# Performance work log

Hardware: AMD Instinct MI355X
Metric: run time of the kernel (lower is better)

Reference implementation:

```python
import jax, jax.numpy as jnp
import numpy as np

NUM_NODES = 100000
OUT_CHANNELS = 32
NUM_EDGES = 3200000


def setup_inputs() -> dict:
    key = jax.random.key(0)
    k1, k2, k3 = jax.random.split(key, 3)
    edge_index = jax.random.randint(k1, (2, NUM_EDGES), 0, NUM_NODES, dtype=jnp.int64)
    # nn.Linear init: weight [out, in], uniform(-1/sqrt(in), 1/sqrt(in))
    bound = 1.0 / np.sqrt(NUM_NODES)
    W = jax.random.uniform(k2, (OUT_CHANNELS, NUM_NODES), jnp.float32, -bound, bound)
    b = jax.random.uniform(k3, (OUT_CHANNELS,), jnp.float32, -bound, bound)
    return {"edge_index": edge_index, "W": W, "b": b}


def reference(edge_index, W, b):
    # LINK forward: A = sparse COO [N, num_nodes] with 1.0 per edge (duplicates sum),
    # logits = A @ W.T + b. Implemented as gather + segment_sum (no dense A).
    row = edge_index[0]
    col = edge_index[1]
    row = row - row.min()  # faithful to `row = row - row.min()`
    gathered = jnp.take(W.T, col, axis=0)  # [E, out_channels]
    logits = jax.ops.segment_sum(gathered, row, num_segments=NUM_NODES)  # [N, out]
    return logits + b
```

## Files before the change

kernel.cpp:

```cpp
#include <hip/hip_runtime.h>

#define NUM_NODES 100000
#define OUT_CH 32
#define NUM_EDGES 3200000

#define RPB 128
#define NB 782
#define NBG 783
#define CAP2 5120
#define FTPB 1024
#define TRB 782
#define BINB 250
#define TILE 12800
#define TPB 512

static __device__ __forceinline__ unsigned short f32_to_bf16_rne(float f) {
    unsigned u = __float_as_uint(f);
    unsigned r = u + 0x7FFFu + ((u >> 16) & 1u);
    return (unsigned short)(r >> 16);
}
static __device__ __forceinline__ float bf16_to_f32(unsigned short h) {
    return __uint_as_float(((unsigned)h) << 16);
}

__global__ void __launch_bounds__(FTPB)
fused_pre(const float* __restrict__ W, ushort4* __restrict__ Wt,
          const int* __restrict__ edge, int* __restrict__ partmin,
          int* __restrict__ bcount, unsigned int* __restrict__ bin) {
    int bk = blockIdx.x;
    int t  = threadIdx.x;
    if (bk < TRB) {
        __shared__ float tile[32][129];
        int tx = t & 127, ty = t >> 7;
        int colBase = bk * 128;
        int col = colBase + tx;
        if (col < NUM_NODES) {
            #pragma unroll
            for (int k = 0; k < 4; k++) {
                int c = ty + 8 * k;
                tile[c][tx] = W[(size_t)c * NUM_NODES + col];
            }
        }
        __syncthreads();
        int lc = t >> 3, q = t & 7;
        int ocol = colBase + lc;
        if (ocol < NUM_NODES) {
            ushort4 o;
            o.x = f32_to_bf16_rne(tile[q * 4 + 0][lc]);
            o.y = f32_to_bf16_rne(tile[q * 4 + 1][lc]);
            o.z = f32_to_bf16_rne(tile[q * 4 + 2][lc]);
            o.w = f32_to_bf16_rne(tile[q * 4 + 3][lc]);
            Wt[(size_t)ocol * 8 + q] = o;
        }
    } else {
        int mb = bk - TRB;
        __shared__ int cnt[NB];
        __shared__ int cur[NB];
        __shared__ int wm[16];
        for (int i = t; i < NB; i += FTPB) cnt[i] = 0;
        __syncthreads();
        int base = mb * TILE;
        int rm = 0x7fffffff;
        for (int o = t; o < TILE; o += FTPB) {
            int r = edge[base + o];
            rm = min(rm, r);
            atomicAdd(&cnt[r >> 7], 1);
        }
        #pragma unroll
        for (int off = 32; off > 0; off >>= 1) rm = min(rm, __shfl_down(rm, off, 64));
        if ((t & 63) == 0) wm[t >> 6] = rm;
        __syncthreads();
        if (t == 0) {
            int m = wm[0];
            #pragma unroll
            for (int w = 1; w < 16; w++) m = min(m, wm[w]);
            partmin[mb] = m;
        }
        for (int i = t; i < NB; i += FTPB)
            cur[i] = cnt[i] ? atomicAdd(&bcount[i], cnt[i]) : 0;
        __syncthreads();
        for (int o = t; o < TILE; o += FTPB) {
            int r = edge[base + o];
            int c = edge[NUM_EDGES + base + o];
            int b = r >> 7;
            int pos = atomicAdd(&cur[b], 1);
            if (pos < CAP2)
                bin[(size_t)b * CAP2 + pos] = ((unsigned)(r & 127) << 17) | (unsigned)c;
        }
    }
}

__global__ void __launch_bounds__(TPB)
bucket_gather(const unsigned int* __restrict__ bin, const int* __restrict__ bcount,
              const int* __restrict__ partmin,
              const ushort4* __restrict__ Wt, const float* __restrict__ b,
              float* __restrict__ out) {
    __shared__ int cnt2[RPB * 8];
    __shared__ int cur2[RPB * 8];
    __shared__ int rowstart[RPB];
    __shared__ int rowcnt[RPB];
    __shared__ int scn[RPB];
    __shared__ int lcol[CAP2];
    __shared__ int wmin[8];
    __shared__ int rminS;

    int t = threadIdx.x;
    int bk = blockIdx.x;
    int pm = (t < BINB) ? partmin[t] : 0x7fffffff;
    #pragma unroll
    for (int off = 32; off > 0; off >>= 1) pm = min(pm, __shfl_down(pm, off, 64));
    if ((t & 63) == 0) wmin[t >> 6] = pm;

    int n = (bk < NB) ? bcount[bk] : 0;
    if (n > CAP2) n = CAP2;
    const unsigned int* mybin = bin + (size_t)bk * CAP2;

    for (int i = t; i < RPB * 8; i += TPB) cnt2[i] = 0;
    __syncthreads();
    if (t == 0) {
        int m = wmin[0];
        #pragma unroll
        for (int w = 1; w < 8; w++) m = min(m, wmin[w]);
        rminS = m;
    }

    for (int i = t; i < n; i += TPB) {
        unsigned int p = mybin[i];
        int lr  = p >> 17;
        int seg = (p & 0x1FFFF) >> 14;
        atomicAdd(&cnt2[(lr << 3) | seg], 1);
    }
    __syncthreads();

    if (t < RPB) {
        int s = 0;
        #pragma unroll
        for (int k = 0; k < 8; k++) s += cnt2[(t << 3) | k];
        rowcnt[t] = s;
        scn[t] = s;
    }
    __syncthreads();
    for (int off = 1; off < RPB; off <<= 1) {
        int v = (t < RPB && t >= off) ? scn[t - off] : 0;
        __syncthreads();
        if (t < RPB) scn[t] += v;
        __syncthreads();
    }
    if (t < RPB) {
        int rs = scn[t] - rowcnt[t];
        rowstart[t] = rs;
        int run = rs;
        #pragma unroll
        for (int k = 0; k < 8; k++) { cur2[(t << 3) | k] = run; run += cnt2[(t << 3) | k]; }
    }
    __syncthreads();

    for (int i = t; i < n; i += TPB) {
        unsigned int p = mybin[i];
        int lr = p >> 17;
        int c  = p & 0x1FFFF;
        int pos = atomicAdd(&cur2[(lr << 3) | (c >> 14)], 1);
        lcol[pos] = c;
    }
    __syncthreads();

    int g   = t >> 3;
    int sub = t & 7;
    float4 bias = ((const float4*)b)[sub];
    int rmin = rminS;
    int lrA = g, lrB = g + 64;
    int outA = bk * RPB + lrA - rmin;
    int outB = bk * RPB + lrB - rmin;
    bool vA = (unsigned)outA < NUM_NODES;
    bool vB = (unsigned)outB < NUM_NODES;
    int iA = rowstart[lrA], eA = iA + rowcnt[lrA];
    int iB = rowstart[lrB], eB = iB + rowcnt[lrB];
    if (!vA) { iA = eA = 0; }
    if (!vB) { iB = eB = 0; }
    float4 accA = bias, accB = bias;
    int nPair = min(eA - iA, eB - iB);
    int k = 0;
    for (; k + 2 <= nPair; k += 2) {
        int cA0 = lcol[iA + k],     cB0 = lcol[iB + k];
        int cA1 = lcol[iA + k + 1], cB1 = lcol[iB + k + 1];
        ushort4 wA0 = Wt[(size_t)cA0 * 8 + sub];
        ushort4 wB0 = Wt[(size_t)cB0 * 8 + sub];
        ushort4 wA1 = Wt[(size_t)cA1 * 8 + sub];
        ushort4 wB1 = Wt[(size_t)cB1 * 8 + sub];
        accA.x += bf16_to_f32(wA0.x) + bf16_to_f32(wA1.x);
        accA.y += bf16_to_f32(wA0.y) + bf16_to_f32(wA1.y);
        accA.z += bf16_to_f32(wA0.z) + bf16_to_f32(wA1.z);
        accA.w += bf16_to_f32(wA0.w) + bf16_to_f32(wA1.w);
        accB.x += bf16_to_f32(wB0.x) + bf16_to_f32(wB1.x);
        accB.y += bf16_to_f32(wB0.y) + bf16_to_f32(wB1.y);
        accB.z += bf16_to_f32(wB0.z) + bf16_to_f32(wB1.z);
        accB.w += bf16_to_f32(wB0.w) + bf16_to_f32(wB1.w);
    }
    for (; k < nPair; k++) {
        ushort4 wA = Wt[(size_t)lcol[iA + k] * 8 + sub];
        ushort4 wB = Wt[(size_t)lcol[iB + k] * 8 + sub];
        accA.x += bf16_to_f32(wA.x); accA.y += bf16_to_f32(wA.y);
        accA.z += bf16_to_f32(wA.z); accA.w += bf16_to_f32(wA.w);
        accB.x += bf16_to_f32(wB.x); accB.y += bf16_to_f32(wB.y);
        accB.z += bf16_to_f32(wB.z); accB.w += bf16_to_f32(wB.w);
    }
    iA += nPair; iB += nPair;
    for (; iA < eA; iA++) {
        ushort4 w = Wt[(size_t)lcol[iA] * 8 + sub];
        accA.x += bf16_to_f32(w.x); accA.y += bf16_to_f32(w.y);
        accA.z += bf16_to_f32(w.z); accA.w += bf16_to_f32(w.w);
    }
    for (; iB < eB; iB++) {
        ushort4 w = Wt[(size_t)lcol[iB] * 8 + sub];
        accB.x += bf16_to_f32(w.x); accB.y += bf16_to_f32(w.y);
        accB.z += bf16_to_f32(w.z); accB.w += bf16_to_f32(w.w);
    }
    if (vA) ((float4*)out)[(size_t)outA * 8 + sub] = accA;
    if (vB) ((float4*)out)[(size_t)outB * 8 + sub] = accB;
}

extern "C" void kernel_launch(void* const* d_in, const int* in_sizes, int n_in,
                              void* d_out, int out_size, void* d_ws, size_t ws_size,
                              hipStream_t stream) {
    const int*   edge = (const int*)d_in[0];
    const float* W    = (const float*)d_in[1];
    const float* b    = (const float*)d_in[2];
    float* out = (float*)d_out;

    char* ws = (char*)d_ws;
    int*          partmin = (int*)ws;
    int*          bcount  = (int*)(ws + 1024);
    ushort4*      Wt      = (ushort4*)(ws + 8192);
    unsigned int* bin     = (unsigned int*)(ws + 6422528);

    hipMemsetAsync(bcount, 0, NBG * sizeof(int), stream);
    fused_pre<<<TRB + BINB, FTPB, 0, stream>>>(W, Wt, edge, partmin, bcount, bin);
    bucket_gather<<<NBG, TPB, 0, stream>>>(bin, bcount, partmin, Wt, b, out);
}
```

Measured before the change: 181.6 us.

## Fuse preprocessing and bucket gather into one persistent cooperative kernel

Merges the transpose/binning kernel and the bucket-gather kernel into a single cooperative persistent kernel. Blocks loop over work items and are separated by a hand-rolled grid barrier on an atomic counter, with shared memory overlaid through a union. Binning now runs with 512-thread blocks over 512 slices instead of 250 tiles of 1024 threads. The aim is to remove the second launch and its gap. In exchange it adds a grid-wide spin barrier and caps the grid size, which may cut parallelism in the gather phase and in the transpose/binning split.

```diff
diff --git a/kernel.cpp b/kernel.cpp
--- a/kernel.cpp
+++ b/kernel.cpp
@@ -8,11 +8,10 @@
 #define NB 782
 #define NBG 783
 #define CAP2 5120
-#define FTPB 1024
+#define TPB 512
 #define TRB 782
-#define BINB 250
-#define TILE 12800
-#define TPB 512
+#define BINS 512
+#define SLICE 6250
 
 static __device__ __forceinline__ unsigned short f32_to_bf16_rne(float f) {
     unsigned u = __float_as_uint(f);
@@ -23,200 +22,217 @@
     return __uint_as_float(((unsigned)h) << 16);
 }
 
-__global__ void __launch_bounds__(FTPB)
-fused_pre(const float* __restrict__ W, ushort4* __restrict__ Wt,
-          const int* __restrict__ edge, int* __restrict__ partmin,
-          int* __restrict__ bcount, unsigned int* __restrict__ bin) {
-    int bk = blockIdx.x;
-    int t  = threadIdx.x;
-    if (bk < TRB) {
-        __shared__ float tile[32][129];
-        int tx = t & 127, ty = t >> 7;
-        int colBase = bk * 128;
-        int col = colBase + tx;
-        if (col < NUM_NODES) {
-            #pragma unroll
-            for (int k = 0; k < 4; k++) {
-                int c = ty + 8 * k;
-                tile[c][tx] = W[(size_t)c * NUM_NODES + col];
-            }
-        }
-        __syncthreads();
-        int lc = t >> 3, q = t & 7;
-        int ocol = colBase + lc;
-        if (ocol < NUM_NODES) {
-            ushort4 o;
-            o.x = f32_to_bf16_rne(tile[q * 4 + 0][lc]);
-            o.y = f32_to_bf16_rne(tile[q * 4 + 1][lc]);
-            o.z = f32_to_bf16_rne(tile[q * 4 + 2][lc]);
-            o.w = f32_to_bf16_rne(tile[q * 4 + 3][lc]);
-            Wt[(size_t)ocol * 8 + q] = o;
+struct TransLds { float tile[32][129]; };
+struct BinLds   { int cnt[NB]; int cur[NB]; int wm[8]; };
+struct GatherLds {
+    int cnt2[RPB * 8]; int cur2[RPB * 8];
+    int rowstart[RPB]; int rowcnt[RPB]; int scn[RPB];
+    int lcol[CAP2]; int wmin[8];
+};
+union AllLds { TransLds tr; BinLds bn; GatherLds g; };
+
+static __device__ __forceinline__ void grid_barrier(int* bar, int t) {
+    __syncthreads();
+    if (t == 0) {
+        __hip_atomic_fetch_add(bar, 1, __ATOMIC_RELEASE, __HIP_MEMORY_SCOPE_AGENT);
+        while (__hip_atomic_load(bar, __ATOMIC_RELAXED, __HIP_MEMORY_SCOPE_AGENT) < (int)gridDim.x)
+            __builtin_amdgcn_s_sleep(2);
+        __builtin_amdgcn_fence(__ATOMIC_ACQUIRE, "agent");
+    }
+    __syncthreads();
+}
+
+__global__ void __launch_bounds__(TPB, 8)
+link_all(const float* __restrict__ W, ushort4* Wt,
+         const int* __restrict__ edge, int* partmin,
+         int* bcount, unsigned int* bin,
+         const float* __restrict__ bv, float* __restrict__ out,
+         int* bar) {
+    __shared__ AllLds u;
+    int bk   = blockIdx.x;
+    int t    = threadIdx.x;
+    int grid = gridDim.x;
+    int tb0  = (grid >= BINS + 256) ? BINS : (grid >> 1);
+
+    if (bk < tb0) {
+        for (int sl = bk; sl < BINS; sl += tb0) {
+            for (int i = t; i < NB; i += TPB) u.bn.cnt[i] = 0;
+            __syncthreads();
+            int base = sl * SLICE;
+            int rm = 0x7fffffff;
+            for (int o = t; o < SLICE; o += TPB) {
+                int r = edge[base + o];
+                rm = min(rm, r);
+                atomicAdd(&u.bn.cnt[r >> 7], 1);
+            }
+            #pragma unroll
+            for (int off = 32; off > 0; off >>= 1) rm = min(rm, __shfl_down(rm, off, 64));
+            if ((t & 63) == 0) u.bn.wm[t >> 6] = rm;
+            __syncthreads();
+            if (t == 0) {
+                int m = u.bn.wm[0];
+                #pragma unroll
+                for (int w = 1; w < TPB / 64; w++) m = min(m, u.bn.wm[w]);
+                partmin[sl] = m;
+            }
+            for (int i = t; i < NB; i += TPB)
+                u.bn.cur[i] = u.bn.cnt[i] ? atomicAdd(&bcount[i], u.bn.cnt[i]) : 0;
+            __syncthreads();
+            for (int o = t; o < SLICE; o += TPB) {
+                int r = edge[base + o];
+                int c = edge[NUM_EDGES + base + o];
+                int b = r >> 7;
+                int pos = atomicAdd(&u.bn.cur[b], 1);
+                if (pos < CAP2)
+                    bin[(size_t)b * CAP2 + pos] = ((unsigned)(r & 127) << 17) | (unsigned)c;
+            }
+            __syncthreads();
         }
     } else {
-        int mb = bk - TRB;
-        __shared__ int cnt[NB];
-        __shared__ int cur[NB];
-        __shared__ int wm[16];
-        for (int i = t; i < NB; i += FTPB) cnt[i] = 0;
-        __syncthreads();
-        int base = mb * TILE;
-        int rm = 0x7fffffff;
-        for (int o = t; o < TILE; o += FTPB) {
-            int r = edge[base + o];
-            rm = min(rm, r);
-            atomicAdd(&cnt[r >> 7], 1);
-        }
-        #pragma unroll
-        for (int off = 32; off > 0; off >>= 1) rm = min(rm, __shfl_down(rm, off, 64));
-        if ((t & 63) == 0) wm[t >> 6] = rm;
-        __syncthreads();
-        if (t == 0) {
-            int m = wm[0];
-            #pragma unroll
-            for (int w = 1; w < 16; w++) m = min(m, wm[w]);
-            partmin[mb] = m;
-        }
-        for (int i = t; i < NB; i += FTPB)
-            cur[i] = cnt[i] ? atomicAdd(&bcount[i], cnt[i]) : 0;
-        __syncthreads();
-        for (int o = t; o < TILE; o += FTPB) {
-            int r = edge[base + o];
-            int c = edge[NUM_EDGES + base + o];
-            int b = r >> 7;
-            int pos = atomicAdd(&cur[b], 1);
-            if (pos < CAP2)
-                bin[(size_t)b * CAP2 + pos] = ((unsigned)(r & 127) << 17) | (unsigned)c;
-        }
-    }
-}
-
-__global__ void __launch_bounds__(TPB)
-bucket_gather(const unsigned int* __restrict__ bin, const int* __restrict__ bcount,
-              const int* __restrict__ partmin,
-              const ushort4* __restrict__ Wt, const float* __restrict__ b,
-              float* __restrict__ out) {
-    __shared__ int cnt2[RPB * 8];
-    __shared__ int cur2[RPB * 8];
-    __shared__ int rowstart[RPB];
-    __shared__ int rowcnt[RPB];
-    __shared__ int scn[RPB];
-    __shared__ int lcol[CAP2];
-    __shared__ int wmin[8];
-    __shared__ int rminS;
-
-    int t = threadIdx.x;
-    int bk = blockIdx.x;
-    int pm = (t < BINB) ? partmin[t] : 0x7fffffff;
+        int tstride = grid - tb0;
+        for (int tb = bk - tb0; tb < TRB; tb += tstride) {
+            int tx = t & 127, ty = t >> 7;
+            int colBase = tb * 128;
+            int col = colBase + tx;
+            if (col < NUM_NODES) {
+                #pragma unroll
+                for (int k = 0; k < 8; k++) {
+                    int c = ty + 4 * k;
+                    u.tr.tile[c][tx] = W[(size_t)c * NUM_NODES + col];
+                }
+            }
+            __syncthreads();
+            #pragma unroll
+            for (int s = 0; s < 2; s++) {
+                int o  = s * TPB + t;
+                int lc = o >> 3, q = o & 7;
+                int ocol = colBase + lc;
+                if (ocol < NUM_NODES) {
+                    ushort4 w;
+                    w.x = f32_to_bf16_rne(u.tr.tile[q * 4 + 0][lc]);
+                    w.y = f32_to_bf16_rne(u.tr.tile[q * 4 + 1][lc]);
+                    w.z = f32_to_bf16_rne(u.tr.tile[q * 4 + 2][lc]);
+                    w.w = f32_to_bf16_rne(u.tr.tile[q * 4 + 3][lc]);
+                    Wt[(size_t)ocol * 8 + q] = w;
+                }
+            }
+            __syncthreads();
+        }
+    }
+    grid_barrier(bar, t);
+
+    int pm = (t < BINS) ? partmin[t] : 0x7fffffff;
     #pragma unroll
     for (int off = 32; off > 0; off >>= 1) pm = min(pm, __shfl_down(pm, off, 64));
-    if ((t & 63) == 0) wmin[t >> 6] = pm;
-
-    int n = (bk < NB) ? bcount[bk] : 0;
-    if (n > CAP2) n = CAP2;
-    const unsigned int* mybin = bin + (size_t)bk * CAP2;
-
-    for (int i = t; i < RPB * 8; i += TPB) cnt2[i] = 0;
-    __syncthreads();
-    if (t == 0) {
-        int m = wmin[0];
-        #pragma unroll
-        for (int w = 1; w < 8; w++) m = min(m, wmin[w]);
-        rminS = m;
-    }
-
-    for (int i = t; i < n; i += TPB) {
-        unsigned int p = mybin[i];
-        int lr  = p >> 17;
-        int seg = (p & 0x1FFFF) >> 14;
-        atomicAdd(&cnt2[(lr << 3) | seg], 1);
-    }
-    __syncthreads();
-
-    if (t < RPB) {
-        int s = 0;
-        #pragma unroll
-        for (int k = 0; k < 8; k++) s += cnt2[(t << 3) | k];
-        rowcnt[t] = s;
-        scn[t] = s;
-    }
-    __syncthreads();
-    for (int off = 1; off < RPB; off <<= 1) {
-        int v = (t < RPB && t >= off) ? scn[t - off] : 0;
-        __syncthreads();
-        if (t < RPB) scn[t] += v;
-        __syncthreads();
-    }
-    if (t < RPB) {
-        int rs = scn[t] - rowcnt[t];
-        rowstart[t] = rs;
-        int run = rs;
-        #pragma unroll
-        for (int k = 0; k < 8; k++) { cur2[(t << 3) | k] = run; run += cnt2[(t << 3) | k]; }
-    }
-    __syncthreads();
-
-    for (int i = t; i < n; i += TPB) {
-        unsigned int p = mybin[i];
-        int lr = p >> 17;
-        int c  = p & 0x1FFFF;
-        int pos = atomicAdd(&cur2[(lr << 3) | (c >> 14)], 1);
-        lcol[pos] = c;
-    }
-    __syncthreads();
-
-    int g   = t >> 3;
-    int sub = t & 7;
-    float4 bias = ((const float4*)b)[sub];
-    int rmin = rminS;
-    int lrA = g, lrB = g + 64;
-    int outA = bk * RPB + lrA - rmin;
-    int outB = bk * RPB + lrB - rmin;
-    bool vA = (unsigned)outA < NUM_NODES;
-    bool vB = (unsigned)outB < NUM_NODES;
-    int iA = rowstart[lrA], eA = iA + rowcnt[lrA];
-    int iB = rowstart[lrB], eB = iB + rowcnt[lrB];
-    if (!vA) { iA = eA = 0; }
-    if (!vB) { iB = eB = 0; }
-    float4 accA = bias, accB = bias;
-    int nPair = min(eA - iA, eB - iB);
-    int k = 0;
-    for (; k + 2 <= nPair; k += 2) {
-        int cA0 = lcol[iA + k],     cB0 = lcol[iB + k];
-        int cA1 = lcol[iA + k + 1], cB1 = lcol[iB + k + 1];
-        ushort4 wA0 = Wt[(size_t)cA0 * 8 + sub];
-        ushort4 wB0 = Wt[(size_t)cB0 * 8 + sub];
-        ushort4 wA1 = Wt[(size_t)cA1 * 8 + sub];
-        ushort4 wB1 = Wt[(size_t)cB1 * 8 + sub];
-        accA.x += bf16_to_f32(wA0.x) + bf16_to_f32(wA1.x);
-        accA.y += bf16_to_f32(wA0.y) + bf16_to_f32(wA1.y);
-        accA.z += bf16_to_f32(wA0.z) + bf16_to_f32(wA1.z);
-        accA.w += bf16_to_f32(wA0.w) + bf16_to_f32(wA1.w);
-        accB.x += bf16_to_f32(wB0.x) + bf16_to_f32(wB1.x);
-        accB.y += bf16_to_f32(wB0.y) + bf16_to_f32(wB1.y);
-        accB.z += bf16_to_f32(wB0.z) + bf16_to_f32(wB1.z);
-        accB.w += bf16_to_f32(wB0.w) + bf16_to_f32(wB1.w);
-    }
-    for (; k < nPair; k++) {
-        ushort4 wA = Wt[(size_t)lcol[iA + k] * 8 + sub];
-        ushort4 wB = Wt[(size_t)lcol[iB + k] * 8 + sub];
-        accA.x += bf16_to_f32(wA.x); accA.y += bf16_to_f32(wA.y);
-        accA.z += bf16_to_f32(wA.z); accA.w += bf16_to_f32(wA.w);
-        accB.x += bf16_to_f32(wB.x); accB.y += bf16_to_f32(wB.y);
-        accB.z += bf16_to_f32(wB.z); accB.w += bf16_to_f32(wB.w);
-    }
-    iA += nPair; iB += nPair;
-    for (; iA < eA; iA++) {
-        ushort4 w = Wt[(size_t)lcol[iA] * 8 + sub];
-        accA.x += bf16_to_f32(w.x); accA.y += bf16_to_f32(w.y);
-        accA.z += bf16_to_f32(w.z); accA.w += bf16_to_f32(w.w);
-    }
-    for (; iB < eB; iB++) {
-        ushort4 w = Wt[(size_t)lcol[iB] * 8 + sub];
-        accB.x += bf16_to_f32(w.x); accB.y += bf16_to_f32(w.y);
-        accB.z += bf16_to_f32(w.z); accB.w += bf16_to_f32(w.w);
-    }
-    if (vA) ((float4*)out)[(size_t)outA * 8 + sub] = accA;
-    if (vB) ((float4*)out)[(size_t)outB * 8 + sub] = accB;
+    if ((t & 63) == 0) u.g.wmin[t >> 6] = pm;
+    __syncthreads();
+    int rmin = u.g.wmin[0];
+    #pragma unroll
+    for (int w = 1; w < TPB / 64; w++) rmin = min(rmin, u.g.wmin[w]);
+    __syncthreads();
+
+    for (int gb = bk; gb < NBG; gb += grid) {
+        int n = (gb < NB) ? bcount[gb] : 0;
+        if (n > CAP2) n = CAP2;
+        const unsigned int* mybin = bin + (size_t)gb * CAP2;
+
+        for (int i = t; i < RPB * 8; i += TPB) u.g.cnt2[i] = 0;
+        __syncthreads();
+
+        for (int i = t; i < n; i += TPB) {
+            unsigned int p = mybin[i];
+            int lr  = p >> 17;
+            int seg = (p & 0x1FFFF) >> 14;
+            atomicAdd(&u.g.cnt2[(lr << 3) | seg], 1);
+        }
+        __syncthreads();
+
+        if (t < RPB) {
+            int s = 0;
+            #pragma unroll
+            for (int k = 0; k < 8; k++) s += u.g.cnt2[(t << 3) | k];
+            u.g.rowcnt[t] = s;
+            u.g.scn[t] = s;
+        }
+        __syncthreads();
+        for (int off = 1; off < RPB; off <<= 1) {
+            int v = (t < RPB && t >= off) ? u.g.scn[t - off] : 0;
+            __syncthreads();
+            if (t < RPB) u.g.scn[t] += v;
+            __syncthreads();
+        }
+        if (t < RPB) {
+            int rs = u.g.scn[t] - u.g.rowcnt[t];
+            u.g.rowstart[t] = rs;
+            int run = rs;
+            #pragma unroll
+            for (int k = 0; k < 8; k++) { u.g.cur2[(t << 3) | k] = run; run += u.g.cnt2[(t << 3) | k]; }
+        }
+        __syncthreads();
+
+        for (int i = t; i < n; i += TPB) {
+            unsigned int p = mybin[i];
+            int lr = p >> 17;
+            int c  = p & 0x1FFFF;
+            int pos = atomicAdd(&u.g.cur2[(lr << 3) | (c >> 14)], 1);
+            u.g.lcol[pos] = c;
+        }
+        __syncthreads();
+
+        int g   = t >> 3;
+        int sub = t & 7;
+        float4 bias = ((const float4*)bv)[sub];
+        int lrA = g, lrB = g + 64;
+        int outA = gb * RPB + lrA - rmin;
+        int outB = gb * RPB + lrB - rmin;
+        bool vA = (unsigned)outA < NUM_NODES;
+        bool vB = (unsigned)outB < NUM_NODES;
+        int iA = u.g.rowstart[lrA], eA = iA + u.g.rowcnt[lrA];
+        int iB = u.g.rowstart[lrB], eB = iB + u.g.rowcnt[lrB];
+        if (!vA) { iA = eA = 0; }
+        if (!vB) { iB = eB = 0; }
+        float4 accA = bias, accB = bias;
+        int nPair = min(eA - iA, eB - iB);
+        int k = 0;
+        for (; k + 2 <= nPair; k += 2) {
+            int cA0 = u.g.lcol[iA + k],     cB0 = u.g.lcol[iB + k];
+            int cA1 = u.g.lcol[iA + k + 1], cB1 = u.g.lcol[iB + k + 1];
+            ushort4 wA0 = Wt[(size_t)cA0 * 8 + sub];
+            ushort4 wB0 = Wt[(size_t)cB0 * 8 + sub];
+            ushort4 wA1 = Wt[(size_t)cA1 * 8 + sub];
+            ushort4 wB1 = Wt[(size_t)cB1 * 8 + sub];
+            accA.x += bf16_to_f32(wA0.x) + bf16_to_f32(wA1.x);
+            accA.y += bf16_to_f32(wA0.y) + bf16_to_f32(wA1.y);
+            accA.z += bf16_to_f32(wA0.z) + bf16_to_f32(wA1.z);
+            accA.w += bf16_to_f32(wA0.w) + bf16_to_f32(wA1.w);
+            accB.x += bf16_to_f32(wB0.x) + bf16_to_f32(wB1.x);
+            accB.y += bf16_to_f32(wB0.y) + bf16_to_f32(wB1.y);
+            accB.z += bf16_to_f32(wB0.z) + bf16_to_f32(wB1.z);
+            accB.w += bf16_to_f32(wB0.w) + bf16_to_f32(wB1.w);
+        }
+        for (; k < nPair; k++) {
+            ushort4 wA = Wt[(size_t)u.g.lcol[iA + k] * 8 + sub];
+            ushort4 wB = Wt[(size_t)u.g.lcol[iB + k] * 8 + sub];
+            accA.x += bf16_to_f32(wA.x); accA.y += bf16_to_f32(wA.y);
+            accA.z += bf16_to_f32(wA.z); accA.w += bf16_to_f32(wA.w);
+            accB.x += bf16_to_f32(wB.x); accB.y += bf16_to_f32(wB.y);
+            accB.z += bf16_to_f32(wB.z); accB.w += bf16_to_f32(wB.w);
+        }
+        iA += nPair; iB += nPair;
+        for (; iA < eA; iA++) {
+            ushort4 w = Wt[(size_t)u.g.lcol[iA] * 8 + sub];
+            accA.x += bf16_to_f32(w.x); accA.y += bf16_to_f32(w.y);
+            accA.z += bf16_to_f32(w.z); accA.w += bf16_to_f32(w.w);
+        }
+        for (; iB < eB; iB++) {
+            ushort4 w = Wt[(size_t)u.g.lcol[iB] * 8 + sub];
+            accB.x += bf16_to_f32(w.x); accB.y += bf16_to_f32(w.y);
+            accB.z += bf16_to_f32(w.z); accB.w += bf16_to_f32(w.w);
+        }
+        if (vA) ((float4*)out)[(size_t)outA * 8 + sub] = accA;
+        if (vB) ((float4*)out)[(size_t)outB * 8 + sub] = accB;
+        __syncthreads();
+    }
 }
 
 extern "C" void kernel_launch(void* const* d_in, const int* in_sizes, int n_in,
@@ -228,12 +244,24 @@
     float* out = (float*)d_out;
 
     char* ws = (char*)d_ws;
-    int*          partmin = (int*)ws;
-    int*          bcount  = (int*)(ws + 1024);
+    int*          bar     = (int*)ws;
+    int*          partmin = (int*)(ws + 1024);
+    int*          bcount  = (int*)(ws + 4096);
     ushort4*      Wt      = (ushort4*)(ws + 8192);
     unsigned int* bin     = (unsigned int*)(ws + 6422528);
 
-    hipMemsetAsync(bcount, 0, NBG * sizeof(int), stream);
-    fused_pre<<<TRB + BINB, FTPB, 0, stream>>>(W, Wt, edge, partmin, bcount, bin);
-    bucket_gather<<<NBG, TPB, 0, stream>>>(bin, bcount, partmin, Wt, b, out);
-}
+    static int bpc = 0;
+    if (bpc == 0) {
+        hipOccupancyMaxActiveBlocksPerMultiprocessor(&bpc, link_all, TPB, 0);
+        if (bpc < 1) bpc = 1;
+        if (bpc > 4) bpc = 4;
+    }
+    int grid = bpc * 256;
+
+    hipMemsetAsync(ws, 0, 7232, stream);
+    void* args[] = { (void*)&W, (void*)&Wt, (void*)&edge, (void*)&partmin,
+                     (void*)&bcount, (void*)&bin, (void*)&b, (void*)&out,
+                     (void*)&bar };
+    hipLaunchCooperativeKernel((const void*)link_all, dim3(grid), dim3(TPB),
+                               args, 0, stream);
+}
```

New measurement: 258.4 us. 42.2% more time.
